# Kernel optimization log

Hardware: AMD Instinct MI355X
Metric: run time of the kernel (lower is better)

Reference implementation:

```python
import jax, jax.numpy as jnp
import numpy as np

DELTA_VAR = 0.5
DELTA_DIST = 1.5
PULL_W = 1.0
PUSH_W = 1.0
REG_W = 0.001
IGNORE_INDEX = 255
NUM_IDS = 16  # max instance id used in setup; fixed segment count for jit


def setup_inputs() -> dict:
    key = jax.random.key(0)
    k1, k2 = jax.random.split(key)
    B, D, H, W = 8, 32, 512, 512
    pred_embedding = jax.random.normal(k1, (B, D, H, W), dtype=jnp.float32)
    gt_instance = jax.random.randint(k2, (B, H, W), 0, NUM_IDS).astype(jnp.int32)
    valid_mask = jnp.ones((B, H, W), dtype=bool)
    return {"pred_embedding": pred_embedding, "gt_instance": gt_instance, "valid_mask": valid_mask}


def _per_image(emb_hwd, inst_hw, vmask_hw):
    # emb_hwd: [H, W, D]; inst_hw, vmask_hw: [H, W]
    D = emb_hwd.shape[-1]
    e = emb_hwd.reshape(-1, D)                       # [N, D]
    inst = inst_hw.reshape(-1)
    m = (vmask_hw.reshape(-1)) & (inst != IGNORE_INDEX)
    mf = m.astype(e.dtype)
    # route invalid pixels to dummy segment NUM_IDS
    seg = jnp.where(m, inst, NUM_IDS)
    counts = jax.ops.segment_sum(mf, seg, num_segments=NUM_IDS + 1)[:NUM_IDS]      # [K]
    sums = jax.ops.segment_sum(e * mf[:, None], seg, num_segments=NUM_IDS + 1)[:NUM_IDS]  # [K, D]
    valid_id = counts > 0
    n_ids = jnp.sum(valid_id.astype(e.dtype))
    centers = sums / jnp.maximum(counts, 1.0)[:, None]                              # [K, D]
    # ---- pull: per-instance mean of relu(||pix - center|| - delta_var)^2 ----
    centers_full = jnp.concatenate([centers, jnp.zeros((1, D), e.dtype)], axis=0)   # dummy row
    c_pix = centers_full[seg]                                                        # [N, D]
    sq = jnp.sum((e - c_pix) ** 2, axis=-1)
    dist = jnp.sqrt(jnp.where(m, sq, 1.0))
    val = jnp.where(m, jax.nn.relu(dist - DELTA_VAR) ** 2, 0.0)
    per_inst = jax.ops.segment_sum(val, seg, num_segments=NUM_IDS + 1)[:NUM_IDS] / jnp.maximum(counts, 1.0)
    pull = jnp.sum(per_inst * valid_id.astype(e.dtype)) / jnp.maximum(n_ids, 1.0)
    # ---- push: pairwise relu(2*delta_dist - ||ci - cj||)^2, off-diagonal mean ----
    sqm = jnp.sum((centers[:, None, :] - centers[None, :, :]) ** 2, axis=-1)        # [K, K]
    eye = jnp.eye(NUM_IDS, dtype=bool)
    pmask = valid_id[:, None] & valid_id[None, :] & (~eye)
    dm = jnp.sqrt(jnp.where(pmask, sqm, 1.0))
    push_mat = jax.nn.relu(2.0 * DELTA_DIST - dm) ** 2
    n_pairs = jnp.sum(pmask.astype(e.dtype))
    push = jnp.where(n_ids > 1.0, jnp.sum(jnp.where(pmask, push_mat, 0.0)) / jnp.maximum(n_pairs, 1.0), 0.0)
    # ---- reg: mean center norm ----
    csq = jnp.sum(centers ** 2, axis=-1)
    cnorm = jnp.sqrt(jnp.where(valid_id, csq, 1.0))
    reg = jnp.sum(jnp.where(valid_id, cnorm, 0.0)) / jnp.maximum(n_ids, 1.0)
    vb = jnp.any(m).astype(e.dtype)
    return pull * vb, push * vb, reg * vb, vb


def reference(pred_embedding, gt_instance, valid_mask):
    emb = jnp.transpose(pred_embedding, (0, 2, 3, 1))  # [B, H, W, D]
    pulls, pushes, regs, vbs = jax.vmap(_per_image)(emb, gt_instance, valid_mask)
    nvb = jnp.sum(vbs)
    denom = jnp.maximum(nvb, 1.0)
    loss = (PULL_W * jnp.sum(pulls) + PUSH_W * jnp.sum(pushes) + REG_W * jnp.sum(regs)) / denom
    return jnp.where(nvb > 0, loss, 0.0)
```

## Files before the change

kernel.cpp:

```cpp
#include <hip/hip_runtime.h>

typedef _Float16 half4 __attribute__((ext_vector_type(4)));
typedef float f32x4 __attribute__((ext_vector_type(4)));

#define NB 8
#define ND 32
#define NHW (512*512)
#define NK 16
#define IGN 255

#define WS_S   1088
#define O_CNT  0
#define O_VPIX 16
#define O_SUM  32
#define O_CEN  544
#define O_PULL 1056
#define O_PUSH 1072
#define O_REG  1073
#define O_VB   1074
#define O_NID  1075

#define IDP_OFF 65536

#define ATPB 256
#define ABLK 128
#define TILE 256
#define NTILES 8
#define ROWP 260

#define PTPB 256
#define PCHUNKS 256
#define PPIX (NHW / PCHUNKS)

__global__ __launch_bounds__(256) void k_zero(float* __restrict__ ws) {
    int i = blockIdx.x * blockDim.x + threadIdx.x;
    if (i < NB * WS_S) ws[i] = 0.f;
}

__global__ __launch_bounds__(ATPB) void k_accum(const float* __restrict__ pred,
                                                const int* __restrict__ inst,
                                                const unsigned char* __restrict__ msk,
                                                float* __restrict__ ws,
                                                unsigned char* __restrict__ idp) {
    __shared__ __align__(16) float buf[2][ND][ROWP];
    __shared__ float lcnt[NK + 2];
    const int tid = threadIdx.x;
    const int w = tid >> 6, l = tid & 63;
    const int dgrp = w & 1;
    const int phalf = w >> 1;
    const int b = blockIdx.y, chunk = blockIdx.x;

    if (tid < NK + 2) lcnt[tid] = 0.f;

    const size_t img = (size_t)b * NHW;
    const float* pb = pred + (size_t)b * ND * NHW;
    const int base0 = chunk * (NTILES * TILE);

#define STAGE(CUR, T)                                                         \
    {                                                                         \
        const int pix0_ = base0 + (T) * TILE;                                 \
        _Pragma("unroll")                                                     \
        for (int q_ = 0; q_ < 8; ++q_) {                                      \
            const int d_ = 8 * w + q_;                                        \
            const float* src_ = pb + (size_t)d_ * NHW + pix0_ + 4 * l;        \
            __builtin_amdgcn_global_load_lds(                                 \
                (const __attribute__((address_space(1))) unsigned*)src_,      \
                (__attribute__((address_space(3))) unsigned*)&buf[CUR][d_][0],\
                16, 0, 0);                                                    \
        }                                                                     \
    }

#define DECODE(IV, MV, PK, VC)                                                \
    {                                                                         \
        const int ia_[4] = {(IV).x, (IV).y, (IV).z, (IV).w};                  \
        (PK) = 0u;                                                            \
        _Pragma("unroll")                                                     \
        for (int p_ = 0; p_ < 4; ++p_) {                                      \
            const bool m_ = ((((MV) >> (8 * p_)) & 0xffu) != 0u) &&           \
                            (ia_[p_] != IGN);                                 \
            (VC) += m_ ? 1.f : 0.f;                                           \
            const unsigned s_ =                                               \
                (m_ && (unsigned)ia_[p_] < NK) ? (unsigned)ia_[p_] : NK;      \
            (PK) |= s_ << (8 * p_);                                           \
        }                                                                     \
    }

    int4 iv = *(const int4*)(inst + img + base0 + 4 * l);
    unsigned mv = *(const unsigned*)(msk + img + base0 + 4 * l);
    STAGE(0, 0);
    unsigned pk;
    float vcnt = 0.f;
    DECODE(iv, mv, pk, vcnt);
    __syncthreads();

    f32x4 acc = {0.f, 0.f, 0.f, 0.f};
    for (int t = 0; t < NTILES; ++t) {
        const int cur = t & 1;
        int4 iv2;
        unsigned mv2 = 0;
        if (t + 1 < NTILES) {
            const int nb0 = base0 + (t + 1) * TILE;
            iv2 = *(const int4*)(inst + img + nb0 + 4 * l);
            mv2 = *(const unsigned*)(msk + img + nb0 + 4 * l);
            STAGE(cur ^ 1, t + 1);
        }
        if (w == 0) {
            uchar4 pkb = {(unsigned char)(pk & 0xff),
                          (unsigned char)((pk >> 8) & 0xff),
                          (unsigned char)((pk >> 16) & 0xff),
                          (unsigned char)(pk >> 24)};
            *(uchar4*)(idp + img + base0 + t * TILE + 4 * l) = pkb;
            #pragma unroll
            for (int p = 0; p < 4; ++p)
                atomicAdd(&lcnt[(pk >> (8 * p)) & 0xffu], 1.f);
        }
        const int pxoff = phalf * 128;
        #pragma unroll
        for (int kk = 0; kk < 8; ++kk) {
            const f32x4 av = *(const f32x4*)
                &buf[cur][dgrp * 16 + (l & 15)][pxoff + kk * 16 + 4 * (l >> 4)];
            half4 ah;
            #pragma unroll
            for (int e = 0; e < 4; ++e) ah[e] = (_Float16)av[e];
            const int srcl = phalf * 32 + kk * 4 + (l >> 4);
            const unsigned pkk = (unsigned)__shfl((int)pk, srcl);
            half4 bh;
            #pragma unroll
            for (int e = 0; e < 4; ++e)
                bh[e] = (((pkk >> (8 * e)) & 0xffu) == (unsigned)(l & 15))
                            ? (_Float16)1.f : (_Float16)0.f;
            acc = __builtin_amdgcn_mfma_f32_16x16x16f16(ah, bh, acc, 0, 0, 0);
        }
        if (t + 1 < NTILES) DECODE(iv2, mv2, pk, vcnt);
        __syncthreads();
    }
#undef STAGE
#undef DECODE

    float* sc = &buf[0][0][0];
    const int widx = dgrp * 2 + phalf;
    #pragma unroll
    for (int r = 0; r < 4; ++r)
        sc[(widx * 16 + 4 * (l >> 4) + r) * 16 + (l & 15)] = acc[r];
    __syncthreads();

    float* wb = ws + b * WS_S;
    for (int i = tid; i < NK * ND; i += ATPB) {
        const int k = i >> 5, d = i & 31, dg = d >> 4, dr = d & 15;
        const float v = sc[((dg * 2 + 0) * 16 + dr) * 16 + k] +
                        sc[((dg * 2 + 1) * 16 + dr) * 16 + k];
        atomicAdd(&wb[O_SUM + i], v);
    }
    if (tid < NK) atomicAdd(&wb[O_CNT + tid], lcnt[tid]);
    if (w == 0) {
        #pragma unroll
        for (int off = 32; off > 0; off >>= 1) vcnt += __shfl_down(vcnt, off);
        if (l == 0) atomicAdd(&wb[O_VPIX], vcnt);
    }
}

__global__ __launch_bounds__(256) void k_centers(float* __restrict__ ws) {
    __shared__ float lc[NK][ND + 1];
    __shared__ float lcnt[NK];
    __shared__ float rsum[256], rcnt[256];
    const int tid = threadIdx.x;
    float* wb = ws + blockIdx.x * WS_S;

    if (tid < NK) lcnt[tid] = wb[O_CNT + tid];
    __syncthreads();
    for (int i = tid; i < NK * ND; i += 256) {
        int k = i >> 5, d = i & 31;
        float c = wb[O_SUM + i] / fmaxf(lcnt[k], 1.f);
        lc[k][d] = c;
        wb[O_CEN + i] = c;
    }
    __syncthreads();

    const int i = tid >> 4, j = tid & 15;
    const bool pm = (i != j) && (lcnt[i] > 0.f) && (lcnt[j] > 0.f);
    float sq = 0.f;
    #pragma unroll
    for (int d = 0; d < ND; ++d) { float df = lc[i][d] - lc[j][d]; sq += df * df; }
    float dm = sqrtf(pm ? sq : 1.f);
    float r = fmaxf(2.f * 1.5f - dm, 0.f);
    rsum[tid] = pm ? r * r : 0.f;
    rcnt[tid] = pm ? 1.f : 0.f;
    __syncthreads();
    for (int s = 128; s > 0; s >>= 1) {
        if (tid < s) { rsum[tid] += rsum[tid + s]; rcnt[tid] += rcnt[tid + s]; }
        __syncthreads();
    }

    if (tid == 0) {
        float nids = 0.f;
        for (int k = 0; k < NK; ++k) nids += (lcnt[k] > 0.f) ? 1.f : 0.f;
        float push = (nids > 1.f) ? rsum[0] / fmaxf(rcnt[0], 1.f) : 0.f;
        float reg = 0.f;
        for (int k = 0; k < NK; ++k) {
            if (lcnt[k] > 0.f) {
                float cs = 0.f;
                for (int d = 0; d < ND; ++d) cs += lc[k][d] * lc[k][d];
                reg += sqrtf(cs);
            }
        }
        reg /= fmaxf(nids, 1.f);
        wb[O_PUSH] = push;
        wb[O_REG] = reg;
        wb[O_VB] = (wb[O_VPIX] > 0.f) ? 1.f : 0.f;
        wb[O_NID] = nids;
    }
}

__global__ __launch_bounds__(PTPB) void k_pull(const float* __restrict__ pred,
                                               const unsigned char* __restrict__ idp,
                                               float* __restrict__ ws) {
    __shared__ float lc[17][ND + 1];
    __shared__ float lp[2][NK];
    const int tid = threadIdx.x;
    const int b = NB - 1 - blockIdx.y;
    const int chunk = PCHUNKS - 1 - blockIdx.x;
    const int half = (tid >> 5) & 1;
    float* wb = ws + b * WS_S;

    for (int i = tid; i < 17 * ND; i += PTPB)
        lc[i >> 5][i & 31] = (i < NK * ND) ? wb[O_CEN + i] : 0.f;
    if (tid < 2 * NK) ((float*)lp)[tid] = 0.f;
    __syncthreads();

    const size_t img = (size_t)b * NHW;
    const float* pb = pred + (size_t)b * ND * NHW;

    const int pix = chunk * PPIX + 4 * tid;
    const unsigned pk = *(const unsigned*)(idp + img + pix);
    const int id[4] = {(int)(pk & 0xff), (int)((pk >> 8) & 0xff),
                       (int)((pk >> 16) & 0xff), (int)(pk >> 24)};
    float sq[4] = {0.f, 0.f, 0.f, 0.f};
    #pragma unroll 8
    for (int d = 0; d < ND; ++d) {
        const float4 v = *(const float4*)(pb + (size_t)d * NHW + pix);
        float df0 = v.x - lc[id[0]][d];
        float df1 = v.y - lc[id[1]][d];
        float df2 = v.z - lc[id[2]][d];
        float df3 = v.w - lc[id[3]][d];
        sq[0] += df0 * df0; sq[1] += df1 * df1;
        sq[2] += df2 * df2; sq[3] += df3 * df3;
    }
    #pragma unroll
    for (int p = 0; p < 4; ++p) {
        if (id[p] < NK) {
            float r = fmaxf(sqrtf(sq[p]) - 0.5f, 0.f);
            atomicAdd(&lp[half][id[p]], r * r);
        }
    }
    __syncthreads();
    if (tid < NK) atomicAdd(&wb[O_PULL + tid], lp[0][tid] + lp[1][tid]);
}

__global__ void k_final(const float* __restrict__ ws, float* __restrict__ out) {
    const int tid = threadIdx.x;
    float contrib = 0.f, vb = 0.f;
    if (tid < NB) {
        const float* wb = ws + tid * WS_S;
        float nids = wb[O_NID];
        float pull = 0.f;
        for (int k = 0; k < NK; ++k) {
            float c = wb[O_CNT + k];
            if (c > 0.f) pull += wb[O_PULL + k] / fmaxf(c, 1.f);
        }
        pull /= fmaxf(nids, 1.f);
        vb = wb[O_VB];
        contrib = (pull + wb[O_PUSH] + 0.001f * wb[O_REG]) * vb;
    }
    #pragma unroll
    for (int off = 32; off > 0; off >>= 1) {
        contrib += __shfl_down(contrib, off);
        vb += __shfl_down(vb, off);
    }
    if (tid == 0) out[0] = (vb > 0.f) ? contrib / fmaxf(vb, 1.f) : 0.f;
}

extern "C" void kernel_launch(void* const* d_in, const int* in_sizes, int n_in,
                              void* d_out, int out_size, void* d_ws, size_t ws_size,
                              hipStream_t stream) {
    const float* pred = (const float*)d_in[0];
    const int* inst = (const int*)d_in[1];
    const unsigned char* msk = (const unsigned char*)d_in[2];
    float* out = (float*)d_out;
    float* ws = (float*)d_ws;
    unsigned char* idp = (unsigned char*)d_ws + IDP_OFF;

    k_zero<<<(NB * WS_S + 255) / 256, 256, 0, stream>>>(ws);
    dim3 agrid(ABLK, NB);
    k_accum<<<agrid, ATPB, 0, stream>>>(pred, inst, msk, ws, idp);
    k_centers<<<NB, 256, 0, stream>>>(ws);
    dim3 pgrid(PCHUNKS, NB);
    k_pull<<<pgrid, PTPB, 0, stream>>>(pred, idp, ws);
    k_final<<<1, 64, 0, stream>>>(ws, out);
}
```

Measured before the change: 111.1 us.

## Shrink accum tile with XOR-swizzled LDS, fold centers kernel into pull/final

The accumulation kernel now stages 128-pixel tiles over 16 iterations into an unpadded LDS buffer. An XOR swizzle on the column index is meant to avoid bank conflicts, and id loading and decoding are split across waves. The separate centers kernel is removed: pull recomputes centers from sums and counts per block, and the final kernel computes push, reg and pull per image. This saves one launch and shrinks LDS use, at the cost of redundant center division in every pull block and a serial loop over images in the single-block final kernel.

```diff
diff --git a/kernel.cpp b/kernel.cpp
--- a/kernel.cpp
+++ b/kernel.cpp
@@ -13,20 +13,14 @@
 #define O_CNT  0
 #define O_VPIX 16
 #define O_SUM  32
-#define O_CEN  544
 #define O_PULL 1056
-#define O_PUSH 1072
-#define O_REG  1073
-#define O_VB   1074
-#define O_NID  1075
 
 #define IDP_OFF 65536
 
 #define ATPB 256
 #define ABLK 128
-#define TILE 256
-#define NTILES 8
-#define ROWP 260
+#define TILE 128
+#define NTILES 16
 
 #define PTPB 256
 #define PCHUNKS 256
@@ -42,53 +36,61 @@
                                                 const unsigned char* __restrict__ msk,
                                                 float* __restrict__ ws,
                                                 unsigned char* __restrict__ idp) {
-    __shared__ __align__(16) float buf[2][ND][ROWP];
-    __shared__ float lcnt[NK + 2];
+    __shared__ __align__(16) float buf[2][ND][TILE];
+    __shared__ float lcnt[2][NK + 1];
     const int tid = threadIdx.x;
     const int w = tid >> 6, l = tid & 63;
     const int dgrp = w & 1;
     const int phalf = w >> 1;
     const int b = blockIdx.y, chunk = blockIdx.x;
 
-    if (tid < NK + 2) lcnt[tid] = 0.f;
+    if (tid < 2 * (NK + 1)) ((float*)lcnt)[tid] = 0.f;
 
     const size_t img = (size_t)b * NHW;
     const float* pb = pred + (size_t)b * ND * NHW;
     const int base0 = chunk * (NTILES * TILE);
 
-#define STAGE(CUR, T)                                                         \
-    {                                                                         \
-        const int pix0_ = base0 + (T) * TILE;                                 \
-        _Pragma("unroll")                                                     \
-        for (int q_ = 0; q_ < 8; ++q_) {                                      \
-            const int d_ = 8 * w + q_;                                        \
-            const float* src_ = pb + (size_t)d_ * NHW + pix0_ + 4 * l;        \
-            __builtin_amdgcn_global_load_lds(                                 \
-                (const __attribute__((address_space(1))) unsigned*)src_,      \
-                (__attribute__((address_space(3))) unsigned*)&buf[CUR][d_][0],\
-                16, 0, 0);                                                    \
-        }                                                                     \
-    }
-
-#define DECODE(IV, MV, PK, VC)                                                \
-    {                                                                         \
-        const int ia_[4] = {(IV).x, (IV).y, (IV).z, (IV).w};                  \
-        (PK) = 0u;                                                            \
-        _Pragma("unroll")                                                     \
-        for (int p_ = 0; p_ < 4; ++p_) {                                      \
-            const bool m_ = ((((MV) >> (8 * p_)) & 0xffu) != 0u) &&           \
-                            (ia_[p_] != IGN);                                 \
-            (VC) += m_ ? 1.f : 0.f;                                           \
-            const unsigned s_ =                                               \
-                (m_ && (unsigned)ia_[p_] < NK) ? (unsigned)ia_[p_] : NK;      \
-            (PK) |= s_ << (8 * p_);                                           \
-        }                                                                     \
-    }
-
-    int4 iv = *(const int4*)(inst + img + base0 + 4 * l);
-    unsigned mv = *(const unsigned*)(msk + img + base0 + 4 * l);
+#define STAGE(CUR, T)                                                          \
+    {                                                                          \
+        const int tb_ = base0 + (T) * TILE;                                    \
+        _Pragma("unroll")                                                      \
+        for (int q_ = 0; q_ < 4; ++q_) {                                       \
+            const int r0_ = 8 * w + 2 * q_;                                    \
+            const int r_ = r0_ + (l >> 5);                                     \
+            const int col_ = 4 * ((l & 31) ^ (r_ & 7));                        \
+            const float* src_ = pb + (size_t)r_ * NHW + tb_ + col_;            \
+            __builtin_amdgcn_global_load_lds(                                  \
+                (const __attribute__((address_space(1))) unsigned*)src_,       \
+                (__attribute__((address_space(3))) unsigned*)&buf[CUR][r0_][0],\
+                16, 0, 0);                                                     \
+        }                                                                      \
+    }
+
+#define LOADIDS(IV, MV, TB)                                                    \
+    if (l < 16) {                                                              \
+        (IV) = *(const int4*)(inst + img + (TB) + phalf * 64 + 4 * l);         \
+        (MV) = *(const unsigned*)(msk + img + (TB) + phalf * 64 + 4 * l);      \
+    }
+
+#define DECODE(IV, MV, PK, VC)                                                 \
+    if (l < 16) {                                                              \
+        const int ia_[4] = {(IV).x, (IV).y, (IV).z, (IV).w};                   \
+        (PK) = 0u;                                                             \
+        _Pragma("unroll")                                                      \
+        for (int p_ = 0; p_ < 4; ++p_) {                                       \
+            const bool m_ = ((((MV) >> (8 * p_)) & 0xffu) != 0u) &&            \
+                            (ia_[p_] != IGN);                                  \
+            if (dgrp == 0) (VC) += m_ ? 1.f : 0.f;                             \
+            const unsigned s_ =                                                \
+                (m_ && (unsigned)ia_[p_] < NK) ? (unsigned)ia_[p_] : NK;       \
+            (PK) |= s_ << (8 * p_);                                            \
+        }                                                                      \
+    }
+
+    int4 iv; unsigned mv = 0;
+    LOADIDS(iv, mv, base0);
     STAGE(0, 0);
-    unsigned pk;
+    unsigned pk = 0;
     float vcnt = 0.f;
     DECODE(iv, mv, pk, vcnt);
     __syncthreads();
@@ -96,33 +98,32 @@
     f32x4 acc = {0.f, 0.f, 0.f, 0.f};
     for (int t = 0; t < NTILES; ++t) {
         const int cur = t & 1;
-        int4 iv2;
-        unsigned mv2 = 0;
+        const int tb = base0 + t * TILE;
+        int4 iv2; unsigned mv2 = 0;
         if (t + 1 < NTILES) {
-            const int nb0 = base0 + (t + 1) * TILE;
-            iv2 = *(const int4*)(inst + img + nb0 + 4 * l);
-            mv2 = *(const unsigned*)(msk + img + nb0 + 4 * l);
+            LOADIDS(iv2, mv2, base0 + (t + 1) * TILE);
             STAGE(cur ^ 1, t + 1);
         }
-        if (w == 0) {
+        if (dgrp == 0 && l < 16) {
             uchar4 pkb = {(unsigned char)(pk & 0xff),
                           (unsigned char)((pk >> 8) & 0xff),
                           (unsigned char)((pk >> 16) & 0xff),
                           (unsigned char)(pk >> 24)};
-            *(uchar4*)(idp + img + base0 + t * TILE + 4 * l) = pkb;
+            *(uchar4*)(idp + img + tb + phalf * 64 + 4 * l) = pkb;
             #pragma unroll
             for (int p = 0; p < 4; ++p)
-                atomicAdd(&lcnt[(pk >> (8 * p)) & 0xffu], 1.f);
-        }
-        const int pxoff = phalf * 128;
-        #pragma unroll
-        for (int kk = 0; kk < 8; ++kk) {
+                atomicAdd(&lcnt[phalf][(pk >> (8 * p)) & 0xffu], 1.f);
+        }
+        #pragma unroll
+        for (int kk = 0; kk < 4; ++kk) {
+            const int row = dgrp * 16 + (l & 15);
+            const int cb = phalf * 16 + kk * 4 + (l >> 4);
             const f32x4 av = *(const f32x4*)
-                &buf[cur][dgrp * 16 + (l & 15)][pxoff + kk * 16 + 4 * (l >> 4)];
+                (&buf[cur][0][0] + row * TILE + 4 * (cb ^ (row & 7)));
             half4 ah;
             #pragma unroll
             for (int e = 0; e < 4; ++e) ah[e] = (_Float16)av[e];
-            const int srcl = phalf * 32 + kk * 4 + (l >> 4);
+            const int srcl = kk * 4 + (l >> 4);
             const unsigned pkk = (unsigned)__shfl((int)pk, srcl);
             half4 bh;
             #pragma unroll
@@ -131,10 +132,12 @@
                             ? (_Float16)1.f : (_Float16)0.f;
             acc = __builtin_amdgcn_mfma_f32_16x16x16f16(ah, bh, acc, 0, 0, 0);
         }
-        if (t + 1 < NTILES) DECODE(iv2, mv2, pk, vcnt);
+        iv = iv2; mv = mv2;
+        DECODE(iv, mv, pk, vcnt);
         __syncthreads();
     }
 #undef STAGE
+#undef LOADIDS
 #undef DECODE
 
     float* sc = &buf[0][0][0];
@@ -151,63 +154,11 @@
                         sc[((dg * 2 + 1) * 16 + dr) * 16 + k];
         atomicAdd(&wb[O_SUM + i], v);
     }
-    if (tid < NK) atomicAdd(&wb[O_CNT + tid], lcnt[tid]);
-    if (w == 0) {
-        #pragma unroll
-        for (int off = 32; off > 0; off >>= 1) vcnt += __shfl_down(vcnt, off);
+    if (tid < NK) atomicAdd(&wb[O_CNT + tid], lcnt[0][tid] + lcnt[1][tid]);
+    if (w == 0 || w == 2) {
+        #pragma unroll
+        for (int off = 8; off > 0; off >>= 1) vcnt += __shfl_down(vcnt, off);
         if (l == 0) atomicAdd(&wb[O_VPIX], vcnt);
-    }
-}
-
-__global__ __launch_bounds__(256) void k_centers(float* __restrict__ ws) {
-    __shared__ float lc[NK][ND + 1];
-    __shared__ float lcnt[NK];
-    __shared__ float rsum[256], rcnt[256];
-    const int tid = threadIdx.x;
-    float* wb = ws + blockIdx.x * WS_S;
-
-    if (tid < NK) lcnt[tid] = wb[O_CNT + tid];
-    __syncthreads();
-    for (int i = tid; i < NK * ND; i += 256) {
-        int k = i >> 5, d = i & 31;
-        float c = wb[O_SUM + i] / fmaxf(lcnt[k], 1.f);
-        lc[k][d] = c;
-        wb[O_CEN + i] = c;
-    }
-    __syncthreads();
-
-    const int i = tid >> 4, j = tid & 15;
-    const bool pm = (i != j) && (lcnt[i] > 0.f) && (lcnt[j] > 0.f);
-    float sq = 0.f;
-    #pragma unroll
-    for (int d = 0; d < ND; ++d) { float df = lc[i][d] - lc[j][d]; sq += df * df; }
-    float dm = sqrtf(pm ? sq : 1.f);
-    float r = fmaxf(2.f * 1.5f - dm, 0.f);
-    rsum[tid] = pm ? r * r : 0.f;
-    rcnt[tid] = pm ? 1.f : 0.f;
-    __syncthreads();
-    for (int s = 128; s > 0; s >>= 1) {
-        if (tid < s) { rsum[tid] += rsum[tid + s]; rcnt[tid] += rcnt[tid + s]; }
-        __syncthreads();
-    }
-
-    if (tid == 0) {
-        float nids = 0.f;
-        for (int k = 0; k < NK; ++k) nids += (lcnt[k] > 0.f) ? 1.f : 0.f;
-        float push = (nids > 1.f) ? rsum[0] / fmaxf(rcnt[0], 1.f) : 0.f;
-        float reg = 0.f;
-        for (int k = 0; k < NK; ++k) {
-            if (lcnt[k] > 0.f) {
-                float cs = 0.f;
-                for (int d = 0; d < ND; ++d) cs += lc[k][d] * lc[k][d];
-                reg += sqrtf(cs);
-            }
-        }
-        reg /= fmaxf(nids, 1.f);
-        wb[O_PUSH] = push;
-        wb[O_REG] = reg;
-        wb[O_VB] = (wb[O_VPIX] > 0.f) ? 1.f : 0.f;
-        wb[O_NID] = nids;
     }
 }
 
@@ -215,6 +166,7 @@
                                                const unsigned char* __restrict__ idp,
                                                float* __restrict__ ws) {
     __shared__ float lc[17][ND + 1];
+    __shared__ float lcc[NK];
     __shared__ float lp[2][NK];
     const int tid = threadIdx.x;
     const int b = NB - 1 - blockIdx.y;
@@ -222,9 +174,12 @@
     const int half = (tid >> 5) & 1;
     float* wb = ws + b * WS_S;
 
+    if (tid < NK) lcc[tid] = wb[O_CNT + tid];
+    if (tid < 2 * NK) ((float*)lp)[tid] = 0.f;
+    __syncthreads();
     for (int i = tid; i < 17 * ND; i += PTPB)
-        lc[i >> 5][i & 31] = (i < NK * ND) ? wb[O_CEN + i] : 0.f;
-    if (tid < 2 * NK) ((float*)lp)[tid] = 0.f;
+        lc[i >> 5][i & 31] =
+            (i < NK * ND) ? wb[O_SUM + i] / fmaxf(lcc[i >> 5], 1.f) : 0.f;
     __syncthreads();
 
     const size_t img = (size_t)b * NHW;
@@ -257,26 +212,63 @@
 }
 
 __global__ void k_final(const float* __restrict__ ws, float* __restrict__ out) {
+    __shared__ float lc[NK][ND];
+    __shared__ float lcc[NK];
     const int tid = threadIdx.x;
-    float contrib = 0.f, vb = 0.f;
-    if (tid < NB) {
-        const float* wb = ws + tid * WS_S;
-        float nids = wb[O_NID];
-        float pull = 0.f;
-        for (int k = 0; k < NK; ++k) {
-            float c = wb[O_CNT + k];
-            if (c > 0.f) pull += wb[O_PULL + k] / fmaxf(c, 1.f);
-        }
-        pull /= fmaxf(nids, 1.f);
-        vb = wb[O_VB];
-        contrib = (pull + wb[O_PUSH] + 0.001f * wb[O_REG]) * vb;
-    }
-    #pragma unroll
-    for (int off = 32; off > 0; off >>= 1) {
-        contrib += __shfl_down(contrib, off);
-        vb += __shfl_down(vb, off);
-    }
-    if (tid == 0) out[0] = (vb > 0.f) ? contrib / fmaxf(vb, 1.f) : 0.f;
+    float total = 0.f, nvb = 0.f;
+
+    for (int b = 0; b < NB; ++b) {
+        const float* wb = ws + b * WS_S;
+        if (tid < NK) lcc[tid] = wb[O_CNT + tid];
+        __syncthreads();
+        for (int i = tid; i < NK * ND; i += 64)
+            lc[i >> 5][i & 31] = wb[O_SUM + i] / fmaxf(lcc[i >> 5], 1.f);
+        __syncthreads();
+
+        float nids_p = (tid < NK && lcc[tid] > 0.f) ? 1.f : 0.f;
+        float pull_p = (tid < NK && lcc[tid] > 0.f)
+                           ? wb[O_PULL + tid] / fmaxf(lcc[tid], 1.f) : 0.f;
+        float reg_p = 0.f;
+        if (tid < NK && lcc[tid] > 0.f) {
+            float cs = 0.f;
+            for (int d = 0; d < ND; ++d) cs += lc[tid][d] * lc[tid][d];
+            reg_p = sqrtf(cs);
+        }
+        float push_p = 0.f;
+        #pragma unroll
+        for (int q = 0; q < 4; ++q) {
+            const int p = 4 * tid + q, i = p >> 4, j = p & 15;
+            if (i != j && lcc[i] > 0.f && lcc[j] > 0.f) {
+                float sq2 = 0.f;
+                for (int d = 0; d < ND; ++d) {
+                    float df = lc[i][d] - lc[j][d];
+                    sq2 += df * df;
+                }
+                float r = fmaxf(3.f - sqrtf(sq2), 0.f);
+                push_p += r * r;
+            }
+        }
+        #pragma unroll
+        for (int off = 32; off > 0; off >>= 1) {
+            nids_p += __shfl_down(nids_p, off);
+            pull_p += __shfl_down(pull_p, off);
+            reg_p  += __shfl_down(reg_p, off);
+            push_p += __shfl_down(push_p, off);
+        }
+        if (tid == 0) {
+            const float nids = nids_p;
+            const float pull = pull_p / fmaxf(nids, 1.f);
+            const float npairs = nids * nids - nids;
+            const float push =
+                (nids > 1.f) ? push_p / fmaxf(npairs, 1.f) : 0.f;
+            const float reg = reg_p / fmaxf(nids, 1.f);
+            const float vb = (wb[O_VPIX] > 0.f) ? 1.f : 0.f;
+            total += (pull + push + 0.001f * reg) * vb;
+            nvb += vb;
+        }
+        __syncthreads();
+    }
+    if (tid == 0) out[0] = (nvb > 0.f) ? total / fmaxf(nvb, 1.f) : 0.f;
 }
 
 extern "C" void kernel_launch(void* const* d_in, const int* in_sizes, int n_in,
@@ -292,7 +284,6 @@
     k_zero<<<(NB * WS_S + 255) / 256, 256, 0, stream>>>(ws);
     dim3 agrid(ABLK, NB);
     k_accum<<<agrid, ATPB, 0, stream>>>(pred, inst, msk, ws, idp);
-    k_centers<<<NB, 256, 0, stream>>>(ws);
     dim3 pgrid(PCHUNKS, NB);
     k_pull<<<pgrid, PTPB, 0, stream>>>(pred, idp, ws);
     k_final<<<1, 64, 0, stream>>>(ws, out);
```

Result: slower. 136.7 us (+23.0%).

## Fold center computation into pull and final kernels, drop k_centers launch

Applied to the files above, without the earlier changes.

Removes the separate k_centers kernel: each k_pull block now computes the centers itself from the sums and counts, and k_final computes push, reg and the number of ids per image. This saves one kernel launch and its serialisation point, at the cost of redundant center divisions in every pull block. k_pull also halves its grid and processes two 4-pixel groups per thread, raising per-thread memory parallelism while halving the number of blocks.

```diff
diff --git a/kernel.cpp b/kernel.cpp
--- a/kernel.cpp
+++ b/kernel.cpp
@@ -13,12 +13,7 @@
 #define O_CNT  0
 #define O_VPIX 16
 #define O_SUM  32
-#define O_CEN  544
 #define O_PULL 1056
-#define O_PUSH 1072
-#define O_REG  1073
-#define O_VB   1074
-#define O_NID  1075
 
 #define IDP_OFF 65536
 
@@ -29,7 +24,7 @@
 #define ROWP 260
 
 #define PTPB 256
-#define PCHUNKS 256
+#define PCHUNKS 128
 #define PPIX (NHW / PCHUNKS)
 
 __global__ __launch_bounds__(256) void k_zero(float* __restrict__ ws) {
@@ -159,62 +154,11 @@
     }
 }
 
-__global__ __launch_bounds__(256) void k_centers(float* __restrict__ ws) {
-    __shared__ float lc[NK][ND + 1];
-    __shared__ float lcnt[NK];
-    __shared__ float rsum[256], rcnt[256];
-    const int tid = threadIdx.x;
-    float* wb = ws + blockIdx.x * WS_S;
-
-    if (tid < NK) lcnt[tid] = wb[O_CNT + tid];
-    __syncthreads();
-    for (int i = tid; i < NK * ND; i += 256) {
-        int k = i >> 5, d = i & 31;
-        float c = wb[O_SUM + i] / fmaxf(lcnt[k], 1.f);
-        lc[k][d] = c;
-        wb[O_CEN + i] = c;
-    }
-    __syncthreads();
-
-    const int i = tid >> 4, j = tid & 15;
-    const bool pm = (i != j) && (lcnt[i] > 0.f) && (lcnt[j] > 0.f);
-    float sq = 0.f;
-    #pragma unroll
-    for (int d = 0; d < ND; ++d) { float df = lc[i][d] - lc[j][d]; sq += df * df; }
-    float dm = sqrtf(pm ? sq : 1.f);
-    float r = fmaxf(2.f * 1.5f - dm, 0.f);
-    rsum[tid] = pm ? r * r : 0.f;
-    rcnt[tid] = pm ? 1.f : 0.f;
-    __syncthreads();
-    for (int s = 128; s > 0; s >>= 1) {
-        if (tid < s) { rsum[tid] += rsum[tid + s]; rcnt[tid] += rcnt[tid + s]; }
-        __syncthreads();
-    }
-
-    if (tid == 0) {
-        float nids = 0.f;
-        for (int k = 0; k < NK; ++k) nids += (lcnt[k] > 0.f) ? 1.f : 0.f;
-        float push = (nids > 1.f) ? rsum[0] / fmaxf(rcnt[0], 1.f) : 0.f;
-        float reg = 0.f;
-        for (int k = 0; k < NK; ++k) {
-            if (lcnt[k] > 0.f) {
-                float cs = 0.f;
-                for (int d = 0; d < ND; ++d) cs += lc[k][d] * lc[k][d];
-                reg += sqrtf(cs);
-            }
-        }
-        reg /= fmaxf(nids, 1.f);
-        wb[O_PUSH] = push;
-        wb[O_REG] = reg;
-        wb[O_VB] = (wb[O_VPIX] > 0.f) ? 1.f : 0.f;
-        wb[O_NID] = nids;
-    }
-}
-
 __global__ __launch_bounds__(PTPB) void k_pull(const float* __restrict__ pred,
                                                const unsigned char* __restrict__ idp,
                                                float* __restrict__ ws) {
     __shared__ float lc[17][ND + 1];
+    __shared__ float lcc[NK];
     __shared__ float lp[2][NK];
     const int tid = threadIdx.x;
     const int b = NB - 1 - blockIdx.y;
@@ -222,34 +166,53 @@
     const int half = (tid >> 5) & 1;
     float* wb = ws + b * WS_S;
 
+    if (tid < NK) lcc[tid] = wb[O_CNT + tid];
+    if (tid < 2 * NK) ((float*)lp)[tid] = 0.f;
+    __syncthreads();
     for (int i = tid; i < 17 * ND; i += PTPB)
-        lc[i >> 5][i & 31] = (i < NK * ND) ? wb[O_CEN + i] : 0.f;
-    if (tid < 2 * NK) ((float*)lp)[tid] = 0.f;
+        lc[i >> 5][i & 31] =
+            (i < NK * ND) ? wb[O_SUM + i] / fmaxf(lcc[i >> 5], 1.f) : 0.f;
     __syncthreads();
 
     const size_t img = (size_t)b * NHW;
     const float* pb = pred + (size_t)b * ND * NHW;
 
-    const int pix = chunk * PPIX + 4 * tid;
-    const unsigned pk = *(const unsigned*)(idp + img + pix);
-    const int id[4] = {(int)(pk & 0xff), (int)((pk >> 8) & 0xff),
-                       (int)((pk >> 16) & 0xff), (int)(pk >> 24)};
-    float sq[4] = {0.f, 0.f, 0.f, 0.f};
+    const int pixA = chunk * PPIX + 4 * tid;
+    const int pixB = pixA + 1024;
+    const unsigned pkA = *(const unsigned*)(idp + img + pixA);
+    const unsigned pkB = *(const unsigned*)(idp + img + pixB);
+    const int idA[4] = {(int)(pkA & 0xff), (int)((pkA >> 8) & 0xff),
+                        (int)((pkA >> 16) & 0xff), (int)(pkA >> 24)};
+    const int idB[4] = {(int)(pkB & 0xff), (int)((pkB >> 8) & 0xff),
+                        (int)((pkB >> 16) & 0xff), (int)(pkB >> 24)};
+    float sqA[4] = {0.f, 0.f, 0.f, 0.f};
+    float sqB[4] = {0.f, 0.f, 0.f, 0.f};
     #pragma unroll 8
     for (int d = 0; d < ND; ++d) {
-        const float4 v = *(const float4*)(pb + (size_t)d * NHW + pix);
-        float df0 = v.x - lc[id[0]][d];
-        float df1 = v.y - lc[id[1]][d];
-        float df2 = v.z - lc[id[2]][d];
-        float df3 = v.w - lc[id[3]][d];
-        sq[0] += df0 * df0; sq[1] += df1 * df1;
-        sq[2] += df2 * df2; sq[3] += df3 * df3;
+        const float4 vA = *(const float4*)(pb + (size_t)d * NHW + pixA);
+        const float4 vB = *(const float4*)(pb + (size_t)d * NHW + pixB);
+        float a0 = vA.x - lc[idA[0]][d];
+        float a1 = vA.y - lc[idA[1]][d];
+        float a2 = vA.z - lc[idA[2]][d];
+        float a3 = vA.w - lc[idA[3]][d];
+        sqA[0] += a0 * a0; sqA[1] += a1 * a1;
+        sqA[2] += a2 * a2; sqA[3] += a3 * a3;
+        float b0 = vB.x - lc[idB[0]][d];
+        float b1 = vB.y - lc[idB[1]][d];
+        float b2 = vB.z - lc[idB[2]][d];
+        float b3 = vB.w - lc[idB[3]][d];
+        sqB[0] += b0 * b0; sqB[1] += b1 * b1;
+        sqB[2] += b2 * b2; sqB[3] += b3 * b3;
     }
     #pragma unroll
     for (int p = 0; p < 4; ++p) {
-        if (id[p] < NK) {
-            float r = fmaxf(sqrtf(sq[p]) - 0.5f, 0.f);
-            atomicAdd(&lp[half][id[p]], r * r);
+        if (idA[p] < NK) {
+            float r = fmaxf(sqrtf(sqA[p]) - 0.5f, 0.f);
+            atomicAdd(&lp[half][idA[p]], r * r);
+        }
+        if (idB[p] < NK) {
+            float r = fmaxf(sqrtf(sqB[p]) - 0.5f, 0.f);
+            atomicAdd(&lp[half][idB[p]], r * r);
         }
     }
     __syncthreads();
@@ -257,26 +220,63 @@
 }
 
 __global__ void k_final(const float* __restrict__ ws, float* __restrict__ out) {
+    __shared__ float lc[NK][ND];
+    __shared__ float lcc[NK];
     const int tid = threadIdx.x;
-    float contrib = 0.f, vb = 0.f;
-    if (tid < NB) {
-        const float* wb = ws + tid * WS_S;
-        float nids = wb[O_NID];
-        float pull = 0.f;
-        for (int k = 0; k < NK; ++k) {
-            float c = wb[O_CNT + k];
-            if (c > 0.f) pull += wb[O_PULL + k] / fmaxf(c, 1.f);
-        }
-        pull /= fmaxf(nids, 1.f);
-        vb = wb[O_VB];
-        contrib = (pull + wb[O_PUSH] + 0.001f * wb[O_REG]) * vb;
-    }
-    #pragma unroll
-    for (int off = 32; off > 0; off >>= 1) {
-        contrib += __shfl_down(contrib, off);
-        vb += __shfl_down(vb, off);
-    }
-    if (tid == 0) out[0] = (vb > 0.f) ? contrib / fmaxf(vb, 1.f) : 0.f;
+    float total = 0.f, nvb = 0.f;
+
+    for (int b = 0; b < NB; ++b) {
+        const float* wb = ws + b * WS_S;
+        if (tid < NK) lcc[tid] = wb[O_CNT + tid];
+        __syncthreads();
+        for (int i = tid; i < NK * ND; i += 64)
+            lc[i >> 5][i & 31] = wb[O_SUM + i] / fmaxf(lcc[i >> 5], 1.f);
+        __syncthreads();
+
+        float nids_p = (tid < NK && lcc[tid] > 0.f) ? 1.f : 0.f;
+        float pull_p = (tid < NK && lcc[tid] > 0.f)
+                           ? wb[O_PULL + tid] / fmaxf(lcc[tid], 1.f) : 0.f;
+        float reg_p = 0.f;
+        if (tid < NK && lcc[tid] > 0.f) {
+            float cs = 0.f;
+            for (int d = 0; d < ND; ++d) cs += lc[tid][d] * lc[tid][d];
+            reg_p = sqrtf(cs);
+        }
+        float push_p = 0.f;
+        #pragma unroll
+        for (int q = 0; q < 4; ++q) {
+            const int p = 4 * tid + q, i = p >> 4, j = p & 15;
+            if (i != j && lcc[i] > 0.f && lcc[j] > 0.f) {
+                float sq2 = 0.f;
+                for (int d = 0; d < ND; ++d) {
+                    float df = lc[i][d] - lc[j][d];
+                    sq2 += df * df;
+                }
+                float r = fmaxf(3.f - sqrtf(sq2), 0.f);
+                push_p += r * r;
+            }
+        }
+        #pragma unroll
+        for (int off = 32; off > 0; off >>= 1) {
+            nids_p += __shfl_down(nids_p, off);
+            pull_p += __shfl_down(pull_p, off);
+            reg_p  += __shfl_down(reg_p, off);
+            push_p += __shfl_down(push_p, off);
+        }
+        if (tid == 0) {
+            const float nids = nids_p;
+            const float pull = pull_p / fmaxf(nids, 1.f);
+            const float npairs = nids * nids - nids;
+            const float push =
+                (nids > 1.f) ? push_p / fmaxf(npairs, 1.f) : 0.f;
+            const float reg = reg_p / fmaxf(nids, 1.f);
+            const float vb = (wb[O_VPIX] > 0.f) ? 1.f : 0.f;
+            total += (pull + push + 0.001f * reg) * vb;
+            nvb += vb;
+        }
+        __syncthreads();
+    }
+    if (tid == 0) out[0] = (nvb > 0.f) ? total / fmaxf(nvb, 1.f) : 0.f;
 }
 
 extern "C" void kernel_launch(void* const* d_in, const int* in_sizes, int n_in,
@@ -292,7 +292,6 @@
     k_zero<<<(NB * WS_S + 255) / 256, 256, 0, stream>>>(ws);
     dim3 agrid(ABLK, NB);
     k_accum<<<agrid, ATPB, 0, stream>>>(pred, inst, msk, ws, idp);
-    k_centers<<<NB, 256, 0, stream>>>(ws);
     dim3 pgrid(PCHUNKS, NB);
     k_pull<<<pgrid, PTPB, 0, stream>>>(pred, idp, ws);
     k_final<<<1, 64, 0, stream>>>(ws, out);
```

Result: slower. 141.0 us (+27.0%).
